# Kernel tuning notes

Measured on AMD Instinct MI355X. Metric: run time of the kernel, lower is better.

Reference implementation:

```python
import jax, jax.numpy as jnp
import numpy as np

B, N, E = 16, 1024, 256
H, D = 16, 16            # head_num * qkv_dim == embedding_dim
FF = 2 * E               # ff_size = embedding_dim * 2
EPS = 1e-5


def setup_inputs() -> dict:
    key = jax.random.key(0)
    ks = jax.random.split(key, 12)
    s = lambda fan_in: 1.0 / np.sqrt(fan_in)
    return {
        "x":  jax.random.normal(ks[0], (B, N, E), dtype=jnp.float32),
        # attention projections (nn.Linear, bias=False) stored as [in, out]
        "Wq": jax.random.uniform(ks[1], (E, H * D), jnp.float32, -s(E), s(E)),
        "Wk": jax.random.uniform(ks[2], (E, H * D), jnp.float32, -s(E), s(E)),
        "Wv": jax.random.uniform(ks[3], (E, H * D), jnp.float32, -s(E), s(E)),
        "Wo": jax.random.uniform(ks[4], (H * D, E), jnp.float32, -s(H * D), s(H * D)),
        "bo": jax.random.uniform(ks[5], (E,), jnp.float32, -s(H * D), s(H * D)),
        # InstanceNorm1d affine params
        "gamma1": jnp.ones((E,), jnp.float32),
        "beta1":  jnp.zeros((E,), jnp.float32),
        "gamma2": jnp.ones((E,), jnp.float32),
        "beta2":  jnp.zeros((E,), jnp.float32),
        # SwiGLU FFN: Linear(E, 2*FF) -> SwiGLU -> Linear(FF, E)
        "W1": jax.random.uniform(ks[6], (E, 2 * FF), jnp.float32, -s(E), s(E)),
        "b1": jax.random.uniform(ks[7], (2 * FF,), jnp.float32, -s(E), s(E)),
        "W2": jax.random.uniform(ks[8], (FF, E), jnp.float32, -s(FF), s(FF)),
        "b2": jax.random.uniform(ks[9], (E,), jnp.float32, -s(FF), s(FF)),
    }


def _instance_norm(x, gamma, beta):
    # x: [B, N, E]; normalize over N per (batch, channel), biased variance
    mean = jnp.mean(x, axis=1, keepdims=True)
    var = jnp.mean(jnp.square(x - mean), axis=1, keepdims=True)
    return (x - mean) * jax.lax.rsqrt(var + EPS) * gamma + beta


def reference(x, Wq, Wk, Wv, Wo, bo, gamma1, beta1, gamma2, beta2, W1, b1, W2, b2):
    b, n, e = x.shape
    q = (x @ Wq).reshape(b, n, H, D)
    k = (x @ Wk).reshape(b, n, H, D)
    v = (x @ Wv).reshape(b, n, H, D)
    scores = jnp.einsum("bnhd,bmhd->bhnm", q, k) / np.sqrt(D)   # [B,H,N,N]
    weights = jax.nn.softmax(scores, axis=-1)
    attn = jnp.einsum("bhnm,bmhd->bnhd", weights, v).reshape(b, n, H * D)
    mha = attn @ Wo + bo
    h = _instance_norm(mha + x, gamma1, beta1)
    # SwiGLU FFN: chunk -> (x_part, gate); silu(gate) * x_part
    proj = h @ W1 + b1
    x_part, gate = proj[..., :FF], proj[..., FF:]
    ff = (jax.nn.silu(gate) * x_part) @ W2 + b2
    return _instance_norm(h + ff, gamma2, beta2)
```

## Files before the change

### kernel.cpp

```cpp
#include <hip/hip_runtime.h>
#include <stdint.h>

typedef unsigned short u16;
typedef __bf16 bf16x8 __attribute__((ext_vector_type(8)));
typedef float f32x4 __attribute__((ext_vector_type(4)));

__device__ __forceinline__ float bf2f(u16 v){ return __uint_as_float(((unsigned)v)<<16); }
__device__ __forceinline__ u16 f2bf(float f){
  unsigned u = __float_as_uint(f);
  unsigned r = (u + 0x7FFFu + ((u>>16)&1u)) >> 16;
  return (u16)r;
}
__device__ __forceinline__ float fexp2(float x){
#if __has_builtin(__builtin_amdgcn_exp2f)
  return __builtin_amdgcn_exp2f(x);
#else
  return exp2f(x);
#endif
}

__global__ void prep_kernel(const float* __restrict__ x_, u16* __restrict__ xb,
                            const float* __restrict__ Wq, const float* __restrict__ Wk,
                            const float* __restrict__ Wv, const float* __restrict__ Wo,
                            const float* __restrict__ W1, const float* __restrict__ W2,
                            u16* __restrict__ wqkvT, u16* __restrict__ woT,
                            u16* __restrict__ w1T, u16* __restrict__ w2T,
                            float* __restrict__ SS)
{
  int bid = blockIdx.x;
  int t = threadIdx.x;
  if (bid >= 640) {
    int idx = ((bid - 640) * 256 + t) * 8;
    float4 a0 = *(const float4*)(x_ + idx);
    float4 a1 = *(const float4*)(x_ + idx + 4);
    union { u16 u[8]; uint4 v; } pk;
    pk.u[0] = f2bf(a0.x); pk.u[1] = f2bf(a0.y); pk.u[2] = f2bf(a0.z); pk.u[3] = f2bf(a0.w);
    pk.u[4] = f2bf(a1.x); pk.u[5] = f2bf(a1.y); pk.u[6] = f2bf(a1.z); pk.u[7] = f2bf(a1.w);
    *(uint4*)(xb + idx) = pk.v;
    return;
  }
  if (bid < 64) SS[bid * 256 + t] = 0.f;
  __shared__ u16 tile[32][33];
  const float* in; u16* out; int K, N, t2; bool glu = false;
  if (bid < 64)       { in = Wq; out = wqkvT;           K = 256; N = 256;  t2 = bid; }
  else if (bid < 128) { in = Wk; out = wqkvT + 65536;   K = 256; N = 256;  t2 = bid - 64; }
  else if (bid < 192) { in = Wv; out = wqkvT + 131072;  K = 256; N = 256;  t2 = bid - 128; }
  else if (bid < 256) { in = Wo; out = woT;             K = 256; N = 256;  t2 = bid - 192; }
  else if (bid < 512) { in = W1; out = w1T;             K = 256; N = 1024; t2 = bid - 256; glu = true; }
  else                { in = W2; out = w2T;             K = 512; N = 256;  t2 = bid - 512; }
  int ntn = N >> 5;
  int k0 = (t2 / ntn) * 32, n0 = (t2 % ntn) * 32;
  #pragma unroll
  for (int p = 0; p < 4; ++p) {
    int u = t + p * 256; int r = u >> 5, c = u & 31;
    tile[r][c] = f2bf(in[(size_t)(k0 + r) * N + n0 + c]);
  }
  __syncthreads();
  #pragma unroll
  for (int p = 0; p < 4; ++p) {
    int u = t + p * 256; int r = u >> 5, c = u & 31;
    int q = n0 + r;
    int row = glu ? (q < 512 ? 2 * q : 2 * (q - 512) + 1) : q;
    out[(size_t)row * K + k0 + c] = tile[c][r];
  }
}

enum { MODE_QKV = 0, MODE_Y_RES = 1, MODE_GLU = 2 };

template<int MODE, int TN, int RESN, int STATS, int NORMA>
__launch_bounds__(256, 3)
__global__ void gemm_kernel(const u16* __restrict__ A, const u16* __restrict__ BT,
                            int M, int N, int K,
                            const float* __restrict__ bias, const u16* __restrict__ resp,
                            u16* __restrict__ outB,
                            float* __restrict__ ssum, float* __restrict__ ssq,
                            const float* __restrict__ nsum, const float* __restrict__ nsq,
                            const float* __restrict__ ngam, const float* __restrict__ nbet)
{
  constexpr int NJ = TN / 32;
  __shared__ u16 As[128 * 40];
  __shared__ u16 Bs[TN * 40];
  __shared__ float scA[256], sfA[256];
  const int t = threadIdx.x;
  const int m0 = blockIdx.x * 128;
  const int n0 = blockIdx.y * TN;
  const int lane = t & 63;
  const int w = t >> 6;
  const int wm = (w >> 1) * 64;
  const int wn = (w & 1) * (NJ * 16);
  const int fr = lane & 15;
  const int fg = lane >> 4;
  const int bIdx = m0 >> 10;
  const float inv1024 = 1.f / 1024.f;

  if (NORMA) {
    int e = t;
    float mean = nsum[bIdx * 256 + e] * inv1024;
    float var = nsq[bIdx * 256 + e] * inv1024 - mean * mean;
    float rstd = rsqrtf(var + 1e-5f);
    float sc = rstd * ngam[e];
    scA[e] = sc;
    sfA[e] = nbet[e] - mean * sc;
  }

  f32x4 acc[4][NJ];
  #pragma unroll
  for (int i = 0; i < 4; ++i)
    #pragma unroll
    for (int j = 0; j < NJ; ++j)
      acc[i][j] = (f32x4){0.f, 0.f, 0.f, 0.f};

  constexpr int TOT = (128 + TN) * 4;
  for (int k0 = 0; k0 < K; k0 += 32) {
    __syncthreads();
    #pragma unroll
    for (int u = 0; u < TOT / 256; ++u) {
      int uu = t + u * 256;
      if (uu < 512) {
        int row = uu >> 2, cb = uu & 3;
        if (NORMA) {
          union { u16 u[8]; uint4 v; } in, o;
          in.v = *(const uint4*)(A + (size_t)(m0 + row) * K + k0 + cb * 8);
          const float* scp = scA + k0 + cb * 8;
          const float* sfp = sfA + k0 + cb * 8;
          float4 s0 = *(const float4*)scp, s1 = *(const float4*)(scp + 4);
          float4 f0 = *(const float4*)sfp, f1 = *(const float4*)(sfp + 4);
          o.u[0] = f2bf(bf2f(in.u[0]) * s0.x + f0.x);
          o.u[1] = f2bf(bf2f(in.u[1]) * s0.y + f0.y);
          o.u[2] = f2bf(bf2f(in.u[2]) * s0.z + f0.z);
          o.u[3] = f2bf(bf2f(in.u[3]) * s0.w + f0.w);
          o.u[4] = f2bf(bf2f(in.u[4]) * s1.x + f1.x);
          o.u[5] = f2bf(bf2f(in.u[5]) * s1.y + f1.y);
          o.u[6] = f2bf(bf2f(in.u[6]) * s1.z + f1.z);
          o.u[7] = f2bf(bf2f(in.u[7]) * s1.w + f1.w);
          *(uint4*)(As + row * 40 + cb * 8) = o.v;
        } else {
          float4 va = *(const float4*)(A + (size_t)(m0 + row) * K + k0 + cb * 8);
          *(float4*)(As + row * 40 + cb * 8) = va;
        }
      } else {
        int v2 = uu - 512;
        int row = v2 >> 2, cb = v2 & 3;
        float4 vb = *(const float4*)(BT + (size_t)(n0 + row) * K + k0 + cb * 8);
        *(float4*)(Bs + row * 40 + cb * 8) = vb;
      }
    }
    __syncthreads();
    bf16x8 af[4], bfr[NJ];
    #pragma unroll
    for (int i = 0; i < 4; ++i) af[i]  = *(const bf16x8*)(As + (wm + i * 16 + fr) * 40 + fg * 8);
    #pragma unroll
    for (int j = 0; j < NJ; ++j) bfr[j] = *(const bf16x8*)(Bs + (wn + j * 16 + fr) * 40 + fg * 8);
    #pragma unroll
    for (int i = 0; i < 4; ++i)
      #pragma unroll
      for (int j = 0; j < NJ; ++j)
        acc[i][j] = __builtin_amdgcn_mfma_f32_16x16x32_bf16(af[i], bfr[j], acc[i][j], 0, 0, 0);
  }

  #pragma unroll
  for (int j = 0; j < NJ; ++j) {
    int col = n0 + wn + j * 16 + fr;
    float bv = 0.f;
    if (MODE == MODE_Y_RES) bv = bias[col];
    if (MODE == MODE_GLU)   bv = bias[(col >> 1) + ((col & 1) << 9)];
    float scj = 0.f, sfj = 0.f;
    if (RESN == 2) {
      float mean = nsum[bIdx * 256 + col] * inv1024;
      float var = nsq[bIdx * 256 + col] * inv1024 - mean * mean;
      float rstd = rsqrtf(var + 1e-5f);
      scj = rstd * ngam[col];
      sfj = nbet[col] - mean * scj;
    }
    float sj = 0.f, qj = 0.f;
    #pragma unroll
    for (int i = 0; i < 4; ++i) {
      #pragma unroll
      for (int r = 0; r < 4; ++r) {
        int row = m0 + wm + i * 16 + fg * 4 + r;
        float v = acc[i][j][r] + bv;
        if (MODE == MODE_QKV) {
          int which = col >> 8, h = (col >> 4) & 15, d = col & 15;
          int b = row >> 10, ns = row & 1023;
          outB[(size_t)which * 4194304 + (((size_t)(b * 16 + h) * 1024 + ns) * 16 + d)] = f2bf(v);
        } else if (MODE == MODE_Y_RES) {
          size_t idx = (size_t)row * N + col;
          float rv = bf2f(resp[idx]);
          if (RESN == 2) rv = rv * scj + sfj;
          float y = v + rv;
          outB[idx] = f2bf(y);
          if (STATS) { sj += y; qj += y * y; }
        } else {
          float partner = __shfl_xor(v, 1);
          if ((fr & 1) == 0) {
            float g = partner / (1.f + __expf(-partner));
            outB[(size_t)row * 512 + (col >> 1)] = f2bf(g * v);
          }
        }
      }
    }
    if (STATS) {
      sj += __shfl_xor(sj, 16); sj += __shfl_xor(sj, 32);
      qj += __shfl_xor(qj, 16); qj += __shfl_xor(qj, 32);
      if (fg == 0) {
        atomicAdd(&ssum[bIdx * 256 + col], sj);
        atomicAdd(&ssq[bIdx * 256 + col], qj);
      }
    }
  }
}

#define SCALE_L2 0.360673760222241f

__launch_bounds__(512, 4)
__global__ void attn_kernel(const u16* __restrict__ Q, const u16* __restrict__ Kg,
                            const u16* __restrict__ Vg, u16* __restrict__ attn)
{
  __shared__ u16 Ks[2][128 * 24];
  __shared__ u16 Vt[2][16 * 136];
  const int t = threadIdx.x;
  const int bh = blockIdx.x & 255;
  const int qg = blockIdx.x >> 8;
  const int b = bh >> 4, h = bh & 15;
  const size_t base = (size_t)bh * 16384;
  const int w = t >> 6, lane = t & 63;
  const int fr = lane & 15, fg = lane >> 4;
  const int q0 = qg * 128 + w * 16;
  const f32x4 zero4 = (f32x4){0.f, 0.f, 0.f, 0.f};

  const int su = (t & 255) >> 1;
  const int sh = t & 1;
  const bool isK = t < 256;
  const int blk = su >> 5, ii = su & 31;
  const int kpos = blk * 32 + ((ii & 1) ? 16 + (ii >> 1) : (ii >> 1));

  bf16x8 qf = {};
  if (fg < 2) {
    union { u16 u[8]; uint4 v; bf16x8 f; } qt;
    qt.v = *(const uint4*)(Q + base + (size_t)(q0 + fr) * 16 + fg * 8);
    #pragma unroll
    for (int j = 0; j < 8; ++j) qt.u[j] = f2bf(bf2f(qt.u[j]) * SCALE_L2);
    qf = qt.f;
  }

  {
    uint4 pre = isK ? *(const uint4*)(Kg + base + (size_t)su * 16 + sh * 8)
                    : *(const uint4*)(Vg + base + (size_t)su * 16 + sh * 8);
    if (isK) {
      *(uint4*)(&Ks[0][kpos * 24 + sh * 8]) = pre;
    } else {
      union { u16 u[8]; uint4 v; } pk; pk.v = pre;
      #pragma unroll
      for (int j = 0; j < 8; ++j) Vt[0][(sh * 8 + j) * 136 + su] = pk.u[j];
    }
  }
  __syncthreads();

  f32x4 acco = zero4;
  float lsum = 0.f;

  for (int c = 0; c < 8; ++c) {
    uint4 nxt;
    if (c < 7) {
      const size_t off = base + (size_t)((c + 1) * 128 + su) * 16 + sh * 8;
      nxt = isK ? *(const uint4*)(Kg + off) : *(const uint4*)(Vg + off);
    }
    const u16* KsC = Ks[c & 1];
    const u16* VtC = Vt[c & 1];
    #pragma unroll
    for (int sub = 0; sub < 4; ++sub) {
      const int kb = sub * 32;
      bf16x8 kf0 = {}, kf1 = {};
      if (fg < 2) {
        kf0 = *(const bf16x8*)(KsC + (kb + fr) * 24 + fg * 8);
        kf1 = *(const bf16x8*)(KsC + (kb + 16 + fr) * 24 + fg * 8);
      }
      f32x4 s0 = __builtin_amdgcn_mfma_f32_16x16x32_bf16(kf0, qf, zero4, 0, 0, 0);
      f32x4 s1 = __builtin_amdgcn_mfma_f32_16x16x32_bf16(kf1, qf, zero4, 0, 0, 0);
      union { unsigned d[4]; bf16x8 f; } pf;
      #pragma unroll
      for (int r = 0; r < 4; ++r) {
        float p0 = fexp2(s0[r]);
        float p1 = fexp2(s1[r]);
        lsum += p0 + p1;
        pf.d[r] = __builtin_amdgcn_perm(__float_as_uint(p1), __float_as_uint(p0), 0x07060302u);
      }
      bf16x8 vf = *(const bf16x8*)(VtC + fr * 136 + kb + fg * 8);
      acco = __builtin_amdgcn_mfma_f32_16x16x32_bf16(vf, pf.f, acco, 0, 0, 0);
    }
    if (c < 7) {
      if (isK) {
        *(uint4*)(&Ks[(c + 1) & 1][kpos * 24 + sh * 8]) = nxt;
      } else {
        union { u16 u[8]; uint4 v; } pk; pk.v = nxt;
        #pragma unroll
        for (int j = 0; j < 8; ++j) Vt[(c + 1) & 1][(sh * 8 + j) * 136 + su] = pk.u[j];
      }
    }
    __syncthreads();
  }

  lsum += __shfl_xor(lsum, 16);
  lsum += __shfl_xor(lsum, 32);
  float inv = 1.f / lsum;
  #pragma unroll
  for (int r = 0; r < 4; ++r) {
    attn[((size_t)(b * 1024 + q0 + fr)) * 256 + h * 16 + fg * 4 + r] = f2bf(acco[r] * inv);
  }
}

__global__ void apply_kernel(const u16* __restrict__ y, const float* __restrict__ ssum,
                             const float* __restrict__ ssq, const float* __restrict__ gamma,
                             const float* __restrict__ beta, float* __restrict__ outp)
{
  int idx = (blockIdx.x * 256 + threadIdx.x) * 4;
  int e = idx & 255;
  int b = idx >> 18;
  union { u16 u[4]; uint2 v; } in;
  in.v = *(const uint2*)(y + idx);
  float ov[4];
  const float inv = 1.f / 1024.f;
  #pragma unroll
  for (int j = 0; j < 4; ++j) {
    int ej = e + j;
    float mean = ssum[b * 256 + ej] * inv;
    float var = ssq[b * 256 + ej] * inv - mean * mean;
    float rstd = rsqrtf(var + 1e-5f);
    ov[j] = (bf2f(in.u[j]) - mean) * rstd * gamma[ej] + beta[ej];
  }
  *(float4*)(outp + idx) = make_float4(ov[0], ov[1], ov[2], ov[3]);
}

extern "C" void kernel_launch(void* const* d_in, const int* in_sizes, int n_in,
                              void* d_out, int out_size, void* d_ws, size_t ws_size,
                              hipStream_t stream)
{
  const float* x      = (const float*)d_in[0];
  const float* Wq     = (const float*)d_in[1];
  const float* Wk     = (const float*)d_in[2];
  const float* Wv     = (const float*)d_in[3];
  const float* Wo     = (const float*)d_in[4];
  const float* bo     = (const float*)d_in[5];
  const float* gamma1 = (const float*)d_in[6];
  const float* beta1  = (const float*)d_in[7];
  const float* gamma2 = (const float*)d_in[8];
  const float* beta2  = (const float*)d_in[9];
  const float* W1     = (const float*)d_in[10];
  const float* b1     = (const float*)d_in[11];
  const float* W2     = (const float*)d_in[12];
  const float* b2     = (const float*)d_in[13];

  char* ws = (char*)d_ws;
  u16*   WQKVT = (u16*)(ws + 0);
  u16*   WOT   = (u16*)(ws + 393216);
  u16*   W1T   = (u16*)(ws + 524288);
  u16*   W2T   = (u16*)(ws + 1048576);
  float* SS    = (float*)(ws + 1310720);
  float* SSUM1 = SS;
  float* SSQ1  = SS + 4096;
  float* SSUM2 = SS + 8192;
  float* SSQ2  = SS + 12288;
  u16*   xb    = (u16*)(ws + 1376256);
  u16*   Qb    = (u16*)(ws + 9764864);
  u16*   ATTN  = (u16*)(ws + 34930688);
  u16*   Y1    = (u16*)(ws + 9764864);
  u16*   G     = (u16*)(ws + 18153472);
  u16*   Y2    = (u16*)(ws + 34930688);

  prep_kernel<<<2688, 256, 0, stream>>>(x, xb, Wq, Wk, Wv, Wo, W1, W2,
                                        WQKVT, WOT, W1T, W2T, SS);

  gemm_kernel<MODE_QKV, 128, 0, 0, 0><<<dim3(128, 6), 256, 0, stream>>>(
      xb, WQKVT, 16384, 768, 256, nullptr, nullptr, Qb,
      nullptr, nullptr, nullptr, nullptr, nullptr, nullptr);

  attn_kernel<<<2048, 512, 0, stream>>>(Qb, Qb + 4194304, Qb + 8388608, ATTN);

  gemm_kernel<MODE_Y_RES, 64, 1, 1, 0><<<dim3(128, 4), 256, 0, stream>>>(
      ATTN, WOT, 16384, 256, 256, bo, xb, Y1,
      SSUM1, SSQ1, nullptr, nullptr, nullptr, nullptr);

  gemm_kernel<MODE_GLU, 128, 0, 0, 1><<<dim3(128, 8), 256, 0, stream>>>(
      Y1, W1T, 16384, 1024, 256, b1, nullptr, G,
      nullptr, nullptr, SSUM1, SSQ1, gamma1, beta1);

  gemm_kernel<MODE_Y_RES, 64, 2, 1, 0><<<dim3(128, 4), 256, 0, stream>>>(
      G, W2T, 16384, 256, 512, b2, Y1, Y2,
      SSUM2, SSQ2, SSUM1, SSQ1, gamma1, beta1);

  apply_kernel<<<4096, 256, 0, stream>>>(Y2, SSUM2, SSQ2, gamma2, beta2, (float*)d_out);
}
```

Baseline: 215.4 us.

## Use direct global-to-LDS loads in GEMM and attention, pre-transpose V

Replaces the register-staged global-to-shared copies in the GEMM and attention kernels with global_load_lds 16-byte transfers. This means the LDS rows are no longer padded (stride 32/16 instead of 40/24). The QKV GEMM epilogue now writes V in a transposed [d][n] layout, so attention can fill its transposed V tile with vector stores instead of scalar scattered stores. The attention output is written as a single 8-byte store. The intent is to cut VGPR traffic and LDS store instructions. The risk is LDS bank conflicts from the removed padding.

Result: no change. 212.3 us (-1.5%).

```diff
diff --git a/kernel.cpp b/kernel.cpp
--- a/kernel.cpp
+++ b/kernel.cpp
@@ -17,6 +17,11 @@
 #else
   return exp2f(x);
 #endif
+}
+__device__ __forceinline__ void gll16(const u16* g, u16* l){
+  __builtin_amdgcn_global_load_lds(
+      (const __attribute__((address_space(1))) void*)g,
+      (__attribute__((address_space(3))) void*)l, 16, 0, 0);
 }
 
 __global__ void prep_kernel(const float* __restrict__ x_, u16* __restrict__ xb,
@@ -78,8 +83,8 @@
                             const float* __restrict__ ngam, const float* __restrict__ nbet)
 {
   constexpr int NJ = TN / 32;
-  __shared__ u16 As[128 * 40];
-  __shared__ u16 Bs[TN * 40];
+  __shared__ u16 As[128 * 32];
+  __shared__ u16 Bs[TN * 32];
   __shared__ float scA[256], sfA[256];
   const int t = threadIdx.x;
   const int m0 = blockIdx.x * 128;
@@ -92,6 +97,8 @@
   const int fg = lane >> 4;
   const int bIdx = m0 >> 10;
   const float inv1024 = 1.f / 1024.f;
+  const int glr = lane >> 2;
+  const int gcb = (lane & 3) * 8;
 
   if (NORMA) {
     int e = t;
@@ -110,47 +117,40 @@
     for (int j = 0; j < NJ; ++j)
       acc[i][j] = (f32x4){0.f, 0.f, 0.f, 0.f};
 
-  constexpr int TOT = (128 + TN) * 4;
   for (int k0 = 0; k0 < K; k0 += 32) {
     __syncthreads();
-    #pragma unroll
-    for (int u = 0; u < TOT / 256; ++u) {
-      int uu = t + u * 256;
-      if (uu < 512) {
+    if (!NORMA) {
+      size_t arow = (size_t)(m0 + w * 32 + glr);
+      gll16(A + arow * K + k0 + gcb,        As + w * 1024);
+      gll16(A + (arow + 16) * K + k0 + gcb, As + w * 1024 + 512);
+    } else {
+      #pragma unroll
+      for (int u = 0; u < 2; ++u) {
+        int uu = t + u * 256;
         int row = uu >> 2, cb = uu & 3;
-        if (NORMA) {
-          union { u16 u[8]; uint4 v; } in, o;
-          in.v = *(const uint4*)(A + (size_t)(m0 + row) * K + k0 + cb * 8);
-          const float* scp = scA + k0 + cb * 8;
-          const float* sfp = sfA + k0 + cb * 8;
-          float4 s0 = *(const float4*)scp, s1 = *(const float4*)(scp + 4);
-          float4 f0 = *(const float4*)sfp, f1 = *(const float4*)(sfp + 4);
-          o.u[0] = f2bf(bf2f(in.u[0]) * s0.x + f0.x);
-          o.u[1] = f2bf(bf2f(in.u[1]) * s0.y + f0.y);
-          o.u[2] = f2bf(bf2f(in.u[2]) * s0.z + f0.z);
-          o.u[3] = f2bf(bf2f(in.u[3]) * s0.w + f0.w);
-          o.u[4] = f2bf(bf2f(in.u[4]) * s1.x + f1.x);
-          o.u[5] = f2bf(bf2f(in.u[5]) * s1.y + f1.y);
-          o.u[6] = f2bf(bf2f(in.u[6]) * s1.z + f1.z);
-          o.u[7] = f2bf(bf2f(in.u[7]) * s1.w + f1.w);
-          *(uint4*)(As + row * 40 + cb * 8) = o.v;
-        } else {
-          float4 va = *(const float4*)(A + (size_t)(m0 + row) * K + k0 + cb * 8);
-          *(float4*)(As + row * 40 + cb * 8) = va;
-        }
-      } else {
-        int v2 = uu - 512;
-        int row = v2 >> 2, cb = v2 & 3;
-        float4 vb = *(const float4*)(BT + (size_t)(n0 + row) * K + k0 + cb * 8);
-        *(float4*)(Bs + row * 40 + cb * 8) = vb;
-      }
+        union { u16 u[8]; uint4 v; } in, o;
+        in.v = *(const uint4*)(A + (size_t)(m0 + row) * K + k0 + cb * 8);
+        const float* scp = scA + k0 + cb * 8;
+        const float* sfp = sfA + k0 + cb * 8;
+        #pragma unroll
+        for (int q = 0; q < 8; ++q) o.u[q] = f2bf(bf2f(in.u[q]) * scp[q] + sfp[q]);
+        *(uint4*)(As + row * 32 + cb * 8) = o.v;
+      }
+    }
+    if (TN == 128) {
+      size_t brow = (size_t)(n0 + w * 32 + glr);
+      gll16(BT + brow * K + k0 + gcb,        Bs + w * 1024);
+      gll16(BT + (brow + 16) * K + k0 + gcb, Bs + w * 1024 + 512);
+    } else {
+      size_t brow = (size_t)(n0 + w * 16 + glr);
+      gll16(BT + brow * K + k0 + gcb, Bs + w * 512);
     }
     __syncthreads();
     bf16x8 af[4], bfr[NJ];
     #pragma unroll
-    for (int i = 0; i < 4; ++i) af[i]  = *(const bf16x8*)(As + (wm + i * 16 + fr) * 40 + fg * 8);
-    #pragma unroll
-    for (int j = 0; j < NJ; ++j) bfr[j] = *(const bf16x8*)(Bs + (wn + j * 16 + fr) * 40 + fg * 8);
+    for (int i = 0; i < 4; ++i) af[i]  = *(const bf16x8*)(As + (wm + i * 16 + fr) * 32 + fg * 8);
+    #pragma unroll
+    for (int j = 0; j < NJ; ++j) bfr[j] = *(const bf16x8*)(Bs + (wn + j * 16 + fr) * 32 + fg * 8);
     #pragma unroll
     for (int i = 0; i < 4; ++i)
       #pragma unroll
@@ -182,7 +182,12 @@
         if (MODE == MODE_QKV) {
           int which = col >> 8, h = (col >> 4) & 15, d = col & 15;
           int b = row >> 10, ns = row & 1023;
-          outB[(size_t)which * 4194304 + (((size_t)(b * 16 + h) * 1024 + ns) * 16 + d)] = f2bf(v);
+          size_t idx;
+          if (which == 2)
+            idx = (size_t)2 * 4194304 + ((size_t)(b * 16 + h)) * 16384 + d * 1024 + ns;
+          else
+            idx = (size_t)which * 4194304 + (((size_t)(b * 16 + h) * 1024 + ns) * 16 + d);
+          outB[idx] = f2bf(v);
         } else if (MODE == MODE_Y_RES) {
           size_t idx = (size_t)row * N + col;
           float rv = bf2f(resp[idx]);
@@ -216,7 +221,7 @@
 __global__ void attn_kernel(const u16* __restrict__ Q, const u16* __restrict__ Kg,
                             const u16* __restrict__ Vg, u16* __restrict__ attn)
 {
-  __shared__ u16 Ks[2][128 * 24];
+  __shared__ u16 Ks[2][128 * 16];
   __shared__ u16 Vt[2][16 * 136];
   const int t = threadIdx.x;
   const int bh = blockIdx.x & 255;
@@ -227,12 +232,13 @@
   const int fr = lane & 15, fg = lane >> 4;
   const int q0 = qg * 128 + w * 16;
   const f32x4 zero4 = (f32x4){0.f, 0.f, 0.f, 0.f};
-
-  const int su = (t & 255) >> 1;
-  const int sh = t & 1;
   const bool isK = t < 256;
-  const int blk = su >> 5, ii = su & 31;
-  const int kpos = blk * 32 + ((ii & 1) ? 16 + (ii >> 1) : (ii >> 1));
+
+  const int si = lane >> 1;
+  const int halfo = (lane & 1) * 8;
+  const int keyloc = (si < 16) ? (2 * si) : (2 * (si - 16) + 1);
+  const int unit = t - 256;
+  const int vd = unit >> 4, voct = unit & 15;
 
   bf16x8 qf = {};
   if (fg < 2) {
@@ -243,16 +249,11 @@
     qf = qt.f;
   }
 
-  {
-    uint4 pre = isK ? *(const uint4*)(Kg + base + (size_t)su * 16 + sh * 8)
-                    : *(const uint4*)(Vg + base + (size_t)su * 16 + sh * 8);
-    if (isK) {
-      *(uint4*)(&Ks[0][kpos * 24 + sh * 8]) = pre;
-    } else {
-      union { u16 u[8]; uint4 v; } pk; pk.v = pre;
-      #pragma unroll
-      for (int j = 0; j < 8; ++j) Vt[0][(sh * 8 + j) * 136 + su] = pk.u[j];
-    }
+  if (isK) {
+    gll16(Kg + base + (size_t)(32 * w + keyloc) * 16 + halfo, &Ks[0][0] + w * 512);
+  } else {
+    uint4 v = *(const uint4*)(Vg + base + vd * 1024 + voct * 8);
+    *(uint4*)(&Vt[0][vd * 136 + voct * 8]) = v;
   }
   __syncthreads();
 
@@ -262,8 +263,11 @@
   for (int c = 0; c < 8; ++c) {
     uint4 nxt;
     if (c < 7) {
-      const size_t off = base + (size_t)((c + 1) * 128 + su) * 16 + sh * 8;
-      nxt = isK ? *(const uint4*)(Kg + off) : *(const uint4*)(Vg + off);
+      if (isK)
+        gll16(Kg + base + (size_t)((c + 1) * 128 + 32 * w + keyloc) * 16 + halfo,
+              &Ks[(c + 1) & 1][0] + w * 512);
+      else
+        nxt = *(const uint4*)(Vg + base + vd * 1024 + (c + 1) * 128 + voct * 8);
     }
     const u16* KsC = Ks[c & 1];
     const u16* VtC = Vt[c & 1];
@@ -272,8 +276,8 @@
       const int kb = sub * 32;
       bf16x8 kf0 = {}, kf1 = {};
       if (fg < 2) {
-        kf0 = *(const bf16x8*)(KsC + (kb + fr) * 24 + fg * 8);
-        kf1 = *(const bf16x8*)(KsC + (kb + 16 + fr) * 24 + fg * 8);
+        kf0 = *(const bf16x8*)(KsC + (kb + fr) * 16 + fg * 8);
+        kf1 = *(const bf16x8*)(KsC + (kb + 16 + fr) * 16 + fg * 8);
       }
       f32x4 s0 = __builtin_amdgcn_mfma_f32_16x16x32_bf16(kf0, qf, zero4, 0, 0, 0);
       f32x4 s1 = __builtin_amdgcn_mfma_f32_16x16x32_bf16(kf1, qf, zero4, 0, 0, 0);
@@ -288,25 +292,18 @@
       bf16x8 vf = *(const bf16x8*)(VtC + fr * 136 + kb + fg * 8);
       acco = __builtin_amdgcn_mfma_f32_16x16x32_bf16(vf, pf.f, acco, 0, 0, 0);
     }
-    if (c < 7) {
-      if (isK) {
-        *(uint4*)(&Ks[(c + 1) & 1][kpos * 24 + sh * 8]) = nxt;
-      } else {
-        union { u16 u[8]; uint4 v; } pk; pk.v = nxt;
-        #pragma unroll
-        for (int j = 0; j < 8; ++j) Vt[(c + 1) & 1][(sh * 8 + j) * 136 + su] = pk.u[j];
-      }
-    }
+    if (c < 7 && !isK)
+      *(uint4*)(&Vt[(c + 1) & 1][vd * 136 + voct * 8]) = nxt;
     __syncthreads();
   }
 
   lsum += __shfl_xor(lsum, 16);
   lsum += __shfl_xor(lsum, 32);
   float inv = 1.f / lsum;
-  #pragma unroll
-  for (int r = 0; r < 4; ++r) {
-    attn[((size_t)(b * 1024 + q0 + fr)) * 256 + h * 16 + fg * 4 + r] = f2bf(acco[r] * inv);
-  }
+  union { u16 u[4]; uint2 v; } ov;
+  #pragma unroll
+  for (int r = 0; r < 4; ++r) ov.u[r] = f2bf(acco[r] * inv);
+  *(uint2*)(attn + ((size_t)(b * 1024 + q0 + fr)) * 256 + h * 16 + fg * 4) = ov.v;
 }
 
 __global__ void apply_kernel(const u16* __restrict__ y, const float* __restrict__ ssum,
```
